# Optimization experiments

Measured on AMD Instinct MI355X. Metric: run time of the kernel, lower is better.

Reference implementation:

```python
import jax, jax.numpy as jnp
import numpy as np


def setup_inputs() -> dict:
    key = jax.random.key(0)
    k1, k2 = jax.random.split(key)
    B, L1, L2, D = 64, 1024, 1024, 768
    sent = jax.random.normal(k1, (B, L1, D), dtype=jnp.float32)
    e = jax.random.normal(k2, (B, L2, L1), dtype=jnp.float32)
    return {"sent": sent, "e": e}


def reference(sent, e):
    # Stable softmax over last axis (alignment weights over L1),
    # then weighted pooling of sent: equivalent to es @ sent.
    es = jax.nn.softmax(e, axis=-1)              # [B, L2, L1]
    out = jnp.einsum('bql,bld->bqd', es, sent)   # [B, L2, D]
    return out
```

## Files before the change

### kernel.cpp

```cpp
#include <hip/hip_runtime.h>
#include <hip/hip_bf16.h>


#define B_  64
#define L1_ 1024
#define L2_ 1024
#define D_  768

typedef __attribute__((ext_vector_type(8))) short short8;
typedef __attribute__((ext_vector_type(4))) float f32x4;
typedef __attribute__((ext_vector_type(8))) unsigned short ushort8;
typedef __attribute__((ext_vector_type(4))) unsigned short ushort4v;

static __device__ __forceinline__ unsigned short f2bf(float x) {
  union { float f; unsigned int u; } c; c.f = x;
  unsigned int r = c.u + 0x7FFF + ((c.u >> 16) & 1);
  return (unsigned short)(r >> 16);
}

#define GLOAD(gp, lp) \
  __builtin_amdgcn_global_load_lds((const __attribute__((address_space(1))) char*)(gp), \
                                   (__attribute__((address_space(3))) char*)(lp), 16, 0, 0)

__global__ __launch_bounds__(256) void transpose_cast_kernel(const float* __restrict__ sent,
                                                             unsigned short* __restrict__ sT) {
  __shared__ unsigned short tile[64][66];
  const int b  = blockIdx.z;
  const int l0 = blockIdx.y << 6;
  const int d0 = blockIdx.x << 6;
  const int t  = threadIdx.x;
  const float* sp = sent + ((size_t)b * L1_ + l0) * D_ + d0;
  const int c4 = (t & 15) << 2;
  const int r0 = t >> 4;
#pragma unroll
  for (int p = 0; p < 4; ++p) {
    const int r = r0 + (p << 4);
    float4 v = *reinterpret_cast<const float4*>(sp + (size_t)r * D_ + c4);
    tile[r][c4 + 0] = f2bf(v.x);
    tile[r][c4 + 1] = f2bf(v.y);
    tile[r][c4 + 2] = f2bf(v.z);
    tile[r][c4 + 3] = f2bf(v.w);
  }
  __syncthreads();
  unsigned short* op = sT + ((size_t)b * D_ + d0) * L1_ + l0;
  const int l8  = (t & 7) << 3;
  const int dd0 = t >> 3;
#pragma unroll
  for (int p = 0; p < 2; ++p) {
    const int d = dd0 + (p << 5);
    ushort8 w;
#pragma unroll
    for (int j = 0; j < 8; ++j) w[j] = tile[l8 + j][d];
    *reinterpret_cast<ushort8*>(op + (size_t)d * L1_ + l8) = w;
  }
}

__global__ __launch_bounds__(256) void exp_rows_kernel(const float* __restrict__ e,
                                                       unsigned short* __restrict__ expE,
                                                       float* __restrict__ rsInv) {
  const int t    = threadIdx.x;
  const int lane = t & 63;
  const int wv   = t >> 6;
  const int rowb = blockIdx.x << 4;
#pragma unroll
  for (int i = 0; i < 4; ++i) {
    const int row = rowb + (i << 2) + wv;
    const float* rp = e + (size_t)row * L1_;
    unsigned short* op = expE + (size_t)row * L1_;
    float s = 0.f;
#pragma unroll
    for (int j = 0; j < 4; ++j) {
      float4 v = *reinterpret_cast<const float4*>(rp + j * 256 + lane * 4);
      float e0 = __expf(v.x), e1 = __expf(v.y), e2 = __expf(v.z), e3 = __expf(v.w);
      s += (e0 + e1) + (e2 + e3);
      ushort4v o;
      o[0] = f2bf(e0); o[1] = f2bf(e1); o[2] = f2bf(e2); o[3] = f2bf(e3);
      *reinterpret_cast<ushort4v*>(op + j * 256 + lane * 4) = o;
    }
#pragma unroll
    for (int dd = 1; dd < 64; dd <<= 1) s += __shfl_xor(s, dd);
    if (lane == 0) rsInv[row] = 1.0f / s;
  }
}

#define BM2 256
#define BN2 256
#define BK2 64
#define NT2   (L1_ / BK2)
#define MT2   (L2_ / BM2)
#define NTL2  (D_ / BN2)
#define NWG2  (B_ * MT2 * NTL2)

#define SA2(T, BUF) do { const int _tt = (T) & (NT2 - 1); \
    _Pragma("unroll") \
    for (int r_ = 0; r_ < 4; ++r_) \
      GLOAD(Asrc2 + (size_t)r_ * 64 * L1_ + _tt * BK2, &As2[BUF][(r_ * 64 + w * 8) * BK2]); \
  } while (0)
#define SB2(T, BUF) do { const int _tt = (T) & (NT2 - 1); \
    _Pragma("unroll") \
    for (int r_ = 0; r_ < 4; ++r_) \
      GLOAD(Bsrc2 + (size_t)r_ * 64 * L1_ + _tt * BK2, &Bs2[BUF][(r_ * 64 + w * 8) * BK2]); \
  } while (0)

#define PHASE2(RB, RH, KH, ...) do { \
    __VA_ARGS__ \
    short8 a_[4], b_[4]; \
    _Pragma("unroll") \
    for (int ii = 0; ii < 4; ++ii) { \
      const int ra_ = wm * 128 + ((RH) * 4 + ii) * 16 + l15; \
      a_[ii] = *reinterpret_cast<const short8*>( \
          &As2[RB][ra_ * BK2 + ((((KH) * 4 + ksl) ^ (l15 & 7)) << 3)]); \
      const int rb_ = wn * 64 + ii * 16 + l15; \
      b_[ii] = *reinterpret_cast<const short8*>( \
          &Bs2[RB][rb_ * BK2 + ((((KH) * 4 + ksl) ^ (l15 & 7)) << 3)]); \
    } \
    __builtin_amdgcn_sched_barrier(0); \
    __builtin_amdgcn_s_barrier(); \
    asm volatile("s_waitcnt lgkmcnt(0)" ::: "memory"); \
    __builtin_amdgcn_sched_barrier(0); \
    __builtin_amdgcn_s_setprio(1); \
    _Pragma("unroll") \
    for (int ii = 0; ii < 4; ++ii) \
      _Pragma("unroll") \
      for (int jj = 0; jj < 4; ++jj) \
        acc[(RH) * 4 + ii][jj] = __builtin_amdgcn_mfma_f32_16x16x32_bf16( \
            a_[ii], b_[jj], acc[(RH) * 4 + ii][jj], 0, 0, 0); \
    __builtin_amdgcn_s_setprio(0); \
    __builtin_amdgcn_sched_barrier(0); \
    __builtin_amdgcn_s_barrier(); \
  } while (0)

#define TILE2(T, RB, SBUF) do { \
    PHASE2(RB, 0, 0, SA2((T) + 1, SBUF); SB2((T) + 1, SBUF); ); \
    PHASE2(RB, 0, 1, ; ); \
    PHASE2(RB, 1, 0, ; ); \
    PHASE2(RB, 1, 1, \
        asm volatile("s_waitcnt vmcnt(0)" ::: "memory"); \
        __builtin_amdgcn_sched_barrier(0); ); \
  } while (0)

__global__ __launch_bounds__(512, 2) void gemm2_kernel(const unsigned short* __restrict__ expE,
                                                       const unsigned short* __restrict__ sT,
                                                       const float* __restrict__ rsInv,
                                                       float* __restrict__ out) {
  __shared__ __align__(16) unsigned short As2[2][BM2 * BK2];
  __shared__ __align__(16) unsigned short Bs2[2][BN2 * BK2];
  __shared__ float sArr[BM2];

  const int orig = blockIdx.x;
  const int wgid = (orig & 7) * (NWG2 / 8) + (orig >> 3);
  const int b    = wgid / (MT2 * NTL2);
  const int rem  = wgid % (MT2 * NTL2);
  const int m0   = (rem / NTL2) * BM2;
  const int n0   = (rem % NTL2) * BN2;

  const int t    = threadIdx.x;
  const int lane = t & 63;
  const int w    = t >> 6;
  const int wm   = w >> 2;
  const int wn   = w & 3;
  const int l15  = lane & 15;
  const int ksl  = lane >> 4;

  const int srow  = w * 8 + (lane >> 3);
  const int sslot = (lane & 7) ^ (lane >> 3);
  const unsigned short* Asrc2 = expE + ((size_t)b * L2_ + m0 + srow) * L1_ + sslot * 8;
  const unsigned short* Bsrc2 = sT   + ((size_t)b * D_  + n0 + srow) * L1_ + sslot * 8;

  if (t < BM2) sArr[t] = rsInv[(size_t)b * L2_ + m0 + t];

  f32x4 acc[8][4] = {};

  SA2(0, 0); SB2(0, 0);
  asm volatile("s_waitcnt vmcnt(0) lgkmcnt(0)" ::: "memory");
  __builtin_amdgcn_s_barrier();
  __builtin_amdgcn_sched_barrier(0);

#pragma unroll 1
  for (int kt = 0; kt < NT2; kt += 2) {
    TILE2(kt,     0, 1);
    TILE2(kt + 1, 1, 0);
  }

  const int rbase = (lane >> 4) << 2;
  float* Cb = out + ((size_t)b * L2_ + m0 + wm * 128) * D_ + n0 + wn * 64;
#pragma unroll
  for (int i = 0; i < 8; ++i) {
    float inv[4];
#pragma unroll
    for (int r = 0; r < 4; ++r)
      inv[r] = sArr[wm * 128 + i * 16 + rbase + r];
#pragma unroll
    for (int jj = 0; jj < 4; ++jj)
#pragma unroll
      for (int r = 0; r < 4; ++r)
        Cb[(size_t)(i * 16 + rbase + r) * D_ + jj * 16 + l15] = acc[i][jj][r] * inv[r];
  }
}

#define BM 128
#define BN 256
#define BK 32
#define NT    (L1_ / BK)
#define NTILE (D_ / BN)
#define MTILE (L2_ / BM)
#define NWG   (NTILE * MTILE * B_)

#define SW(r) ((((r) >> 2) ^ (r)) & 3)

#define LOADA(T) do { const int _ta = (T) & (NT - 1);                                        \
    aregs[0] = *reinterpret_cast<const float4*>(Ae + (size_t)rA * L1_ + _ta * BK + cA);      \
    aregs[1] = *reinterpret_cast<const float4*>(Ae + (size_t)rA * L1_ + _ta * BK + cA + 4);  \
  } while (0)

#define EXPWRITE(T) do { if ((T) < NT) {                                        \
    unsigned short* Ad_ = &As[(T) & 1][0];                                      \
    float ex_[8];                                                               \
    ex_[0] = __expf(aregs[0].x); ex_[1] = __expf(aregs[0].y);                   \
    ex_[2] = __expf(aregs[0].z); ex_[3] = __expf(aregs[0].w);                   \
    ex_[4] = __expf(aregs[1].x); ex_[5] = __expf(aregs[1].y);                   \
    ex_[6] = __expf(aregs[1].z); ex_[7] = __expf(aregs[1].w);                   \
    psum += ((ex_[0] + ex_[1]) + (ex_[2] + ex_[3]))                             \
          + ((ex_[4] + ex_[5]) + (ex_[6] + ex_[7]));                            \
    ushort8 w0_;                                                                \
    _Pragma("unroll")                                                           \
    for (int q_ = 0; q_ < 8; ++q_) w0_[q_] = f2bf(ex_[q_]);                     \
    *reinterpret_cast<ushort8*>(&Ad_[rA * BK + aslot * 8]) = w0_;               \
  } } while (0)

#define SB(T) do { if ((T) < NT) {                                              \
    GLOAD(Bb + (size_t)rB0 * L1_ + (T) * BK + sB0, &Bs[(T) & 1][(w * 32) * BK]);      \
    GLOAD(Bb + (size_t)rB1 * L1_ + (T) * BK + sB1, &Bs[(T) & 1][(w * 32 + 16) * BK]); \
  } } while (0)

__global__ __launch_bounds__(512, 2) void gemm_fused_kernel(const float* __restrict__ e,
                                                            const unsigned short* __restrict__ sT,
                                                            float* __restrict__ out) {
  __shared__ __align__(16) unsigned short As[2][BM * BK];
  __shared__ __align__(16) unsigned short Bs[2][BN * BK];
  __shared__ float sArr[BM];

  const int orig = blockIdx.x;
  const int wgid = (orig & 7) * (NWG / 8) + (orig >> 3);
  const int b    = wgid / (NTILE * MTILE);
  const int rem  = wgid % (NTILE * MTILE);
  const int m0   = (rem / NTILE) * BM;
  const int n0   = (rem % NTILE) * BN;

  const int t    = threadIdx.x;
  const int lane = t & 63;
  const int w    = t >> 6;
  const int wm   = w >> 2;
  const int wn   = w & 3;
  const int l15  = lane & 15;
  const int ksl  = lane >> 4;
  const int rA   = w * 16 + (lane >> 2);
  const int cA   = (lane & 3) * 8;
  const int aslot = (lane & 3) ^ SW(rA);
  const int rB0  = w * 32 + (lane >> 2);
  const int rB1  = rB0 + 16;
  const int sB0  = ((lane & 3) ^ SW(rB0)) * 8;
  const int sB1  = ((lane & 3) ^ SW(rB1)) * 8;

  const float*          Ae = e  + ((size_t)b * L2_ + m0) * L1_;
  const unsigned short* Bb = sT + ((size_t)b * D_  + n0) * L1_;

  f32x4 acc[4][4] = {};
  float4 aregs[2];
  float psum = 0.f;

  LOADA(0);
  SB(0);
  EXPWRITE(0);
  LOADA(1);
  asm volatile("s_waitcnt vmcnt(2) lgkmcnt(0)" ::: "memory");
  __builtin_amdgcn_s_barrier();
  __builtin_amdgcn_sched_barrier(0);

  for (int kt = 0; kt < NT; ++kt) {
    SB(kt + 1);
    EXPWRITE(kt + 1);
    LOADA(kt + 2);

    const unsigned short* Apt = As[kt & 1];
    const unsigned short* Bpt = Bs[kt & 1];
    short8 a[4], bb[4];
    __builtin_amdgcn_s_setprio(1);
#pragma unroll
    for (int i = 0; i < 4; ++i) {
      const int ra = wm * 64 + i * 16 + l15;
      a[i] = *reinterpret_cast<const short8*>(&Apt[ra * BK + ((ksl ^ SW(ra)) << 3)]);
      const int rb = wn * 64 + i * 16 + l15;
      bb[i] = *reinterpret_cast<const short8*>(&Bpt[rb * BK + ((ksl ^ SW(rb)) << 3)]);
    }
#pragma unroll
    for (int i = 0; i < 4; ++i)
#pragma unroll
      for (int jn = 0; jn < 4; ++jn)
        acc[i][jn] = __builtin_amdgcn_mfma_f32_16x16x32_bf16(a[i], bb[jn], acc[i][jn], 0, 0, 0);
    __builtin_amdgcn_s_setprio(0);

    if (kt < NT - 1) {
      asm volatile("s_waitcnt vmcnt(2) lgkmcnt(0)" ::: "memory");
      __builtin_amdgcn_s_barrier();
      __builtin_amdgcn_sched_barrier(0);
    }
  }

  psum += __shfl_xor(psum, 1);
  psum += __shfl_xor(psum, 2);
  if ((lane & 3) == 0) sArr[rA] = psum;
  __syncthreads();

  const int rbase = (lane >> 4) << 2;
  float* Cb = out + ((size_t)b * L2_ + m0 + wm * 64) * D_ + n0 + wn * 64;
#pragma unroll
  for (int i = 0; i < 4; ++i) {
    float inv[4];
#pragma unroll
    for (int r = 0; r < 4; ++r)
      inv[r] = 1.0f / sArr[wm * 64 + i * 16 + rbase + r];
#pragma unroll
    for (int jn = 0; jn < 4; ++jn)
#pragma unroll
      for (int r = 0; r < 4; ++r)
        Cb[(size_t)(i * 16 + rbase + r) * D_ + jn * 16 + l15] = acc[i][jn][r] * inv[r];
  }
}

extern "C" void kernel_launch(void* const* d_in, const int* in_sizes, int n_in,
                              void* d_out, int out_size, void* d_ws, size_t ws_size,
                              hipStream_t stream) {
  const float* sent = (const float*)d_in[0];
  const float* e    = (const float*)d_in[1];
  float* out = (float*)d_out;

  const size_t ST_BYTES   = (size_t)B_ * D_ * L1_ * 2;
  const size_t EXPE_BYTES = (size_t)B_ * L2_ * L1_ * 2;
  const size_t RS_BYTES   = (size_t)B_ * L2_ * 4;

  unsigned short* sT = (unsigned short*)d_ws;

  transpose_cast_kernel<<<dim3(D_ / 64, L1_ / 64, B_), 256, 0, stream>>>(sent, sT);

  if (ws_size >= ST_BYTES + EXPE_BYTES + RS_BYTES) {
    unsigned short* expE  = (unsigned short*)((char*)d_ws + ST_BYTES);
    float*          rsInv = (float*)((char*)d_ws + ST_BYTES + EXPE_BYTES);
    exp_rows_kernel<<<dim3(B_ * L2_ / 16), 256, 0, stream>>>(e, expE, rsInv);
    gemm2_kernel<<<dim3(NWG2), 512, 0, stream>>>(expE, sT, rsInv, out);
  } else {
    gemm_fused_kernel<<<dim3(NWG), 512, 0, stream>>>(e, sT, out);
  }
}
```

Measured before the change: 296.3 us.

## Spread tile prefetch loads across phases and prefetch A half-tiles two ahead

Global-to-LDS loads for the next K tile are now split into pairs of row blocks and issued across the four MFMA phases instead of all in the first phase. The A rows used only by the first half of the phases are prefetched two tiles ahead into the current buffer, once those rows have been consumed. The wait before the tile switch becomes vmcnt(2), so those early loads can stay in flight. This aims to hide more memory latency and smooth out issue bursts, at the cost of tighter buffer-reuse reasoning and some risk of LDS races.

```diff
diff --git a/kernel.cpp b/kernel.cpp
--- a/kernel.cpp
+++ b/kernel.cpp
@@ -91,19 +91,21 @@
 #define NTL2  (D_ / BN2)
 #define NWG2  (B_ * MT2 * NTL2)
 
-#define SA2(T, BUF) do { const int _tt = (T) & (NT2 - 1); \
-    _Pragma("unroll") \
-    for (int r_ = 0; r_ < 4; ++r_) \
-      GLOAD(Asrc2 + (size_t)r_ * 64 * L1_ + _tt * BK2, &As2[BUF][(r_ * 64 + w * 8) * BK2]); \
-  } while (0)
-#define SB2(T, BUF) do { const int _tt = (T) & (NT2 - 1); \
-    _Pragma("unroll") \
-    for (int r_ = 0; r_ < 4; ++r_) \
-      GLOAD(Bsrc2 + (size_t)r_ * 64 * L1_ + _tt * BK2, &Bs2[BUF][(r_ * 64 + w * 8) * BK2]); \
-  } while (0)
-
-#define PHASE2(RB, RH, KH, ...) do { \
-    __VA_ARGS__ \
+#define SAU(T, BUF, RR) do { const int _tt = (T) & (NT2 - 1); \
+    GLOAD(Asrc2 + (size_t)(RR) * 64 * L1_ + _tt * BK2, \
+          &As2[BUF][((RR) * 64 + w * 8) * BK2]); \
+    GLOAD(Asrc2 + (size_t)((RR) + 2) * 64 * L1_ + _tt * BK2, \
+          &As2[BUF][(((RR) + 2) * 64 + w * 8) * BK2]); \
+  } while (0)
+#define SBU(T, BUF, RR) do { const int _tt = (T) & (NT2 - 1); \
+    GLOAD(Bsrc2 + (size_t)(RR) * 64 * L1_ + _tt * BK2, \
+          &Bs2[BUF][((RR) * 64 + w * 8) * BK2]); \
+    GLOAD(Bsrc2 + (size_t)((RR) + 1) * 64 * L1_ + _tt * BK2, \
+          &Bs2[BUF][(((RR) + 1) * 64 + w * 8) * BK2]); \
+  } while (0)
+
+#define PHASE2(RB, RH, KH, PRE, POST) do { \
+    PRE \
     short8 a_[4], b_[4]; \
     _Pragma("unroll") \
     for (int ii = 0; ii < 4; ++ii) { \
@@ -126,17 +128,18 @@
         acc[(RH) * 4 + ii][jj] = __builtin_amdgcn_mfma_f32_16x16x32_bf16( \
             a_[ii], b_[jj], acc[(RH) * 4 + ii][jj], 0, 0, 0); \
     __builtin_amdgcn_s_setprio(0); \
+    POST \
     __builtin_amdgcn_sched_barrier(0); \
     __builtin_amdgcn_s_barrier(); \
   } while (0)
 
 #define TILE2(T, RB, SBUF) do { \
-    PHASE2(RB, 0, 0, SA2((T) + 1, SBUF); SB2((T) + 1, SBUF); ); \
-    PHASE2(RB, 0, 1, ; ); \
-    PHASE2(RB, 1, 0, ; ); \
-    PHASE2(RB, 1, 1, \
-        asm volatile("s_waitcnt vmcnt(0)" ::: "memory"); \
-        __builtin_amdgcn_sched_barrier(0); ); \
+    PHASE2(RB, 0, 0, SAU((T) + 1, SBUF, 1);, ;); \
+    PHASE2(RB, 0, 1, SBU((T) + 1, SBUF, 0);, ;); \
+    PHASE2(RB, 1, 0, SBU((T) + 1, SBUF, 2); SAU((T) + 2, RB, 0);, ;); \
+    PHASE2(RB, 1, 1, ;, \
+        asm volatile("s_waitcnt vmcnt(2)" ::: "memory"); \
+        __builtin_amdgcn_sched_barrier(0);); \
   } while (0)
 
 __global__ __launch_bounds__(512, 2) void gemm2_kernel(const unsigned short* __restrict__ expE,
@@ -167,12 +170,12 @@
   const unsigned short* Asrc2 = expE + ((size_t)b * L2_ + m0 + srow) * L1_ + sslot * 8;
   const unsigned short* Bsrc2 = sT   + ((size_t)b * D_  + n0 + srow) * L1_ + sslot * 8;
 
+  f32x4 acc[8][4] = {};
+
   if (t < BM2) sArr[t] = rsInv[(size_t)b * L2_ + m0 + t];
-
-  f32x4 acc[8][4] = {};
-
-  SA2(0, 0); SB2(0, 0);
-  asm volatile("s_waitcnt vmcnt(0) lgkmcnt(0)" ::: "memory");
+  SAU(0, 0, 0); SAU(0, 0, 1); SBU(0, 0, 0); SBU(0, 0, 2);
+  SAU(1, 1, 0);
+  asm volatile("s_waitcnt vmcnt(2) lgkmcnt(0)" ::: "memory");
   __builtin_amdgcn_s_barrier();
   __builtin_amdgcn_sched_barrier(0);
 
```

After: 302.5 us. 1.02x slower.
